# Kernel tuning notes

Measured on AMD Instinct MI355X. Metric: run time of the kernel, lower is better.

The kernel has to match this reference:

```python
import jax, jax.numpy as jnp
import numpy as np

N = 524288   # total graph nodes
V = 64       # number of virtual nodes (clusters)
C = N // V   # nodes per cluster (8192)
D = 256      # in_feats
H = 256      # hidden_feats
EPS = 1e-5


def setup_inputs() -> dict:
    key = jax.random.key(0)
    ks = jax.random.split(key, 8)
    sD = 1.0 / np.sqrt(D)
    sH = 1.0 / np.sqrt(2 * H)
    inp = {
        "x": jax.random.normal(ks[0], (N, D), dtype=jnp.float32),
        "vn_emb": jax.random.normal(ks[1], (V, D), dtype=jnp.float32) * 0.1,
        "wq": jax.random.normal(ks[2], (D, D), dtype=jnp.float32) * sD,
        "wk": jax.random.normal(ks[3], (D, D), dtype=jnp.float32) * sD,
        "v_attn": jax.random.normal(ks[4], (D,), dtype=jnp.float32) * sD,
        "w1": jax.random.normal(ks[5], (D, 2 * H), dtype=jnp.float32) * sD,
        "b1": jnp.zeros((2 * H,), dtype=jnp.float32),
        "g1": jnp.ones((2 * H,), dtype=jnp.float32),
        "beta1": jnp.zeros((2 * H,), dtype=jnp.float32),
        "w2": jax.random.normal(ks[6], (2 * H, H), dtype=jnp.float32) * sH,
        "b2": jnp.zeros((H,), dtype=jnp.float32),
        "g2": jnp.ones((H,), dtype=jnp.float32),
        "beta2": jnp.zeros((H,), dtype=jnp.float32),
        # cluster v owns contiguous node block [v*C, (v+1)*C)
        "vn_index": jnp.arange(N, dtype=jnp.int32).reshape(V, C),
        "vn_indices": jnp.stack(
            [jnp.arange(N, dtype=jnp.int32), (jnp.arange(N, dtype=jnp.int32) // C)],
            axis=1),
    }
    return inp


def _batchnorm(z, g, b):
    # training-mode BN over the virtual-node batch dim
    m = jnp.mean(z, axis=0)
    v = jnp.var(z, axis=0)
    return (z - m) * jax.lax.rsqrt(v + EPS) * g + b


def reference(x, vn_emb, wq, wk, v_attn, w1, b1, g1, beta1,
              w2, b2, g2, beta2, vn_index, vn_indices):
    vx = vn_emb                                   # [V, D]
    # --- update_node_emb (layer 0): broadcast-add VN emb to its nodes ---
    h = x + vx[vn_indices[:, 1]]                  # [N, D]
    # --- update_vn_emb: per-cluster additive attention pooling (vectorized over V) ---
    cluster_h = h[vn_index]                       # [V, C, D]
    q = vx @ wq                                   # [V, D]
    kproj = jnp.einsum('vcd,de->vce', cluster_h, wk)   # [V, C, D]
    scores = jnp.einsum('vce,e->vc', jnp.tanh(kproj + q[:, None, :]), v_attn)
    attn = jax.nn.softmax(scores, axis=-1)        # [V, C]
    pooled = jnp.einsum('vc,vcd->vd', attn, cluster_h) + vx  # [V, D]
    # --- mlp_vns[0]: Linear -> BN -> ReLU -> Linear -> BN -> ReLU ---
    z = jax.nn.relu(_batchnorm(pooled @ w1 + b1, g1, beta1))  # [V, 2H]
    vx_new = jax.nn.relu(_batchnorm(z @ w2 + b2, g2, beta2))  # [V, H]
    return h, vx_new
```

## Files before the change

### kernel.cpp

```cpp
#include <hip/hip_runtime.h>


typedef __bf16 bf16x8 __attribute__((ext_vector_type(8)));
typedef float f32x4 __attribute__((ext_vector_type(4)));
typedef unsigned short us8 __attribute__((ext_vector_type(8)));

__device__ __forceinline__ unsigned short f2bf(float f) {
  unsigned int u = __float_as_uint(f);
  return (unsigned short)((u + 0x7fffu + ((u >> 16) & 1u)) >> 16);
}
__device__ __forceinline__ float bf2f(unsigned short s) {
  return __uint_as_float(((unsigned int)s) << 16);
}
__device__ __forceinline__ float tanh_fast(float x) {
  float cx = fminf(fmaxf(x, -15.f), 15.f);
  float e = __expf(2.f * cx);
  return (e - 1.f) * __builtin_amdgcn_rcpf(e + 1.f);
}
__device__ __forceinline__ float wave_sum(float v) {
#pragma unroll
  for (int o = 1; o < 64; o <<= 1) v += __shfl_xor(v, o);
  return v;
}
__device__ __forceinline__ void lgkm_barrier() {
  asm volatile("s_waitcnt lgkmcnt(0)" ::: "memory");
  __builtin_amdgcn_sched_barrier(0);
  __builtin_amdgcn_s_barrier();
  __builtin_amdgcn_sched_barrier(0);
}

#define PXLD(dst, voff) \
  asm volatile("global_load_dwordx4 %0, %1, %2" : "=v"(dst) : "v"(voff), "s"(x))

__global__ __launch_bounds__(256) void k_prep(
    const float* __restrict__ vn_emb, const float* __restrict__ wq,
    const float* __restrict__ wk, float* __restrict__ qg,
    unsigned short* __restrict__ wkp) {
  int t = threadIdx.x;
  int b = blockIdx.x;
  if (b < 64) {
    float a = 0.f;
#pragma unroll 4
    for (int d = 0; d < 256; ++d) a += vn_emb[(b << 8) + d] * wq[(d << 8) + t];
    qg[(b << 8) + t] = a;
  } else {
    int tid = ((b - 64) << 8) + t;
    int l = tid & 63;
    int ks = (tid >> 6) & 7;
    int ct = tid >> 9;
    int col = (ct << 4) + (l & 15);
    int d0 = (ks << 5) + ((l >> 4) << 3);
    us8 o;
#pragma unroll
    for (int e = 0; e < 8; ++e) o[e] = f2bf(wk[(d0 + e) * 256 + col]);
    *reinterpret_cast<us8*>(wkp + (size_t)tid * 8) = o;
  }
}

__global__ __launch_bounds__(512, 2) void k_main(
    const float* __restrict__ x, const float* __restrict__ vn_emb,
    const float* __restrict__ v_attn, const float* __restrict__ qg,
    const unsigned short* __restrict__ wkp, float* __restrict__ hout,
    float* __restrict__ vecs, float* __restrict__ Zb) {
  __shared__ unsigned short wk_lds[65536];
  __shared__ unsigned short hs[32 * 256];
  __shared__ float vxs[256], qv[256], va[256];
  __shared__ float spbuf[4][32];

  const int t = threadIdx.x;
  const int blk = blockIdx.x;
  const int cl = blk >> 2;

  if (t < 256) {
    vxs[t] = vn_emb[(cl << 8) + t];
    qv[t] = qg[(cl << 8) + t];
    va[t] = v_attn[t];
  }
  {
    const f32x4* wkg = reinterpret_cast<const f32x4*>(wkp);
    f32x4* wkl = reinterpret_cast<f32x4*>(wk_lds);
#pragma unroll
    for (int j = 0; j < 16; ++j) wkl[(j << 9) + t] = wkg[(j << 9) + t];
  }

  const int l = t & 63, wv = t >> 6;
  const int lr = l & 15, lg = l >> 4;
  const int rg = wv & 1, ctq = wv >> 1;

  char* hsb = reinterpret_cast<char*>(hs);
  const unsigned blk_base = (unsigned)blk * 2097152u;
  f32x4* hop = reinterpret_cast<f32x4*>(hout) + ((size_t)blk << 17);

  f32x4 acc = {0.f, 0.f, 0.f, 0.f};
  float zacc = 0.f;

  f32x4 px0, px1, px2, px3;
  {
    unsigned vo = blk_base + ((unsigned)t << 4);
    PXLD(px0, vo);
    PXLD(px1, vo + 8192u);
    PXLD(px2, vo + 16384u);
    PXLD(px3, vo + 24576u);
  }
  __syncthreads();

  for (int tile = 0; tile < 64; ++tile) {
    asm volatile("s_waitcnt vmcnt(0)" ::: "memory");
    __builtin_amdgcn_sched_barrier(0);
    const int tb4 = tile << 11;
#define STAGE1_STEP(i, pxr)                                               \
  {                                                                       \
    int id = (i << 9) + t;                                                \
    int row = id >> 6, c4 = id & 63;                                      \
    f32x4 vv = *reinterpret_cast<const f32x4*>(&vxs[c4 << 2]);            \
    f32x4 hh = pxr + vv;                                                  \
    hop[tb4 + id] = hh;                                                   \
    ushort4 o;                                                            \
    o.x = f2bf(hh[0]);                                                    \
    o.y = f2bf(hh[1]);                                                    \
    o.z = f2bf(hh[2]);                                                    \
    o.w = f2bf(hh[3]);                                                    \
    *reinterpret_cast<ushort4*>(                                          \
        hsb + ((row << 9) + ((c4 << 3) ^ ((row & 7) << 4)))) = o;         \
  }
    STAGE1_STEP(0, px0)
    STAGE1_STEP(1, px1)
    STAGE1_STEP(2, px2)
    STAGE1_STEP(3, px3)
#undef STAGE1_STEP
    lgkm_barrier();

    if (tile < 63) {
      unsigned nvo = blk_base + ((unsigned)(tile + 1) << 15) + ((unsigned)t << 4);
      PXLD(px0, nvo);
      PXLD(px1, nvo + 8192u);
      PXLD(px2, nvo + 16384u);
      PXLD(px3, nvo + 24576u);
    }
    __builtin_amdgcn_sched_barrier(0);

    bf16x8 bfr[8];
    {
      int row2 = (rg << 4) + lr;
      int sw = (row2 & 7) << 4;
#pragma unroll
      for (int ks = 0; ks < 8; ++ks)
        bfr[ks] = __builtin_bit_cast(
            bf16x8, *reinterpret_cast<const us8*>(
                        hsb + ((row2 << 9) + ((((ks << 6) + (lg << 4))) ^ sw))));
    }
    float sp = 0.f;
#pragma unroll
    for (int c = 0; c < 4; ++c) {
      const int ct = (ctq << 2) + c;
      f32x4 ac0 = {0.f, 0.f, 0.f, 0.f};
#pragma unroll
      for (int ks = 0; ks < 8; ++ks) {
        bf16x8 af = __builtin_bit_cast(
            bf16x8, *reinterpret_cast<const us8*>(
                        wk_lds + ((size_t)(((ct << 3) + ks) << 6) + l) * 8));
        ac0 =
            __builtin_amdgcn_mfma_f32_16x16x32_bf16(af, bfr[ks], ac0, 0, 0, 0);
      }
      const int eo0 = (ct << 4) + (lg << 2);
      const f32x4 qf = *reinterpret_cast<const f32x4*>(&qv[eo0]);
      const f32x4 vf = *reinterpret_cast<const f32x4*>(&va[eo0]);
#pragma unroll
      for (int r = 0; r < 4; ++r) sp += tanh_fast(ac0[r] + qf[r]) * vf[r];
    }
    sp += __shfl_xor(sp, 16);
    sp += __shfl_xor(sp, 32);
    if (lg == 0) spbuf[ctq][(rg << 4) + lr] = sp;
    lgkm_barrier();

    float srow = 0.f;
    if (l < 32) srow = spbuf[0][l] + spbuf[1][l] + spbuf[2][l] + spbuf[3][l];
    float w_all = __expf(srow);
    if (wv == 0 && l < 32) zacc += w_all;

#pragma unroll
    for (int r = 0; r < 4; ++r) {
      int row = (wv << 2) + r;
      float wn = __shfl(w_all, row);
      ushort4 hv = *reinterpret_cast<const ushort4*>(
          hsb + ((row << 9) + ((l << 3) ^ ((row & 7) << 4))));
      acc[0] += wn * bf2f(hv.x);
      acc[1] += wn * bf2f(hv.y);
      acc[2] += wn * bf2f(hv.z);
      acc[3] += wn * bf2f(hv.w);
    }
    lgkm_barrier();
  }

  float* sc = reinterpret_cast<float*>(hs);
  *reinterpret_cast<f32x4*>(&sc[(wv << 8) + (l << 2)]) = acc;
  __syncthreads();
  if (t < 256) {
    float s = 0.f;
#pragma unroll
    for (int w8 = 0; w8 < 8; ++w8) s += sc[(w8 << 8) + t];
    vecs[((size_t)blk << 8) + t] = s;
  }
  if (wv == 0) {
    float z = wave_sum(zacc);
    if (l == 0) Zb[blk] = z;
  }
}

__global__ __launch_bounds__(256) void k_combine(
    const float* __restrict__ vecs, const float* __restrict__ Zb,
    const float* __restrict__ vn_emb, float* __restrict__ pooledT) {
  int v = blockIdx.x, t = threadIdx.x;
  float s = 0.f, z = 0.f;
#pragma unroll
  for (int b = 0; b < 4; ++b) {
    s += vecs[(size_t)(((v << 2) + b) << 8) + t];
    z += Zb[(v << 2) + b];
  }
  pooledT[(t << 6) + v] = s / z + vn_emb[(v << 8) + t];
}

__global__ __launch_bounds__(64) void k_mlp1(
    const float* __restrict__ pooledT, const float* __restrict__ w1,
    const float* __restrict__ b1, const float* __restrict__ g1,
    const float* __restrict__ be1, float* __restrict__ z1T) {
  int j = blockIdx.x, v = threadIdx.x;
  float a = 0.f;
#pragma unroll 4
  for (int d = 0; d < 256; ++d) a += pooledT[(d << 6) + v] * w1[(d << 9) + j];
  a += b1[j];
  float mu = wave_sum(a) * (1.f / 64.f);
  float df = a - mu;
  float var = wave_sum(df * df) * (1.f / 64.f);
  float z = df * rsqrtf(var + 1e-5f) * g1[j] + be1[j];
  z1T[(j << 6) + v] = fmaxf(z, 0.f);
}

__global__ __launch_bounds__(64) void k_mlp2(
    const float* __restrict__ z1T, const float* __restrict__ w2,
    const float* __restrict__ b2, const float* __restrict__ g2,
    const float* __restrict__ be2, float* __restrict__ vout) {
  int j = blockIdx.x, v = threadIdx.x;
  float a = 0.f;
#pragma unroll 4
  for (int k = 0; k < 512; ++k) a += z1T[(k << 6) + v] * w2[(k << 8) + j];
  a += b2[j];
  float mu = wave_sum(a) * (1.f / 64.f);
  float df = a - mu;
  float var = wave_sum(df * df) * (1.f / 64.f);
  float z = df * rsqrtf(var + 1e-5f) * g2[j] + be2[j];
  vout[(v << 8) + j] = fmaxf(z, 0.f);
}

extern "C" void kernel_launch(void* const* d_in, const int* in_sizes, int n_in,
                              void* d_out, int out_size, void* d_ws,
                              size_t ws_size, hipStream_t stream) {
  const float* x = (const float*)d_in[0];
  const float* vn_emb = (const float*)d_in[1];
  const float* wq = (const float*)d_in[2];
  const float* wk = (const float*)d_in[3];
  const float* v_attn = (const float*)d_in[4];
  const float* w1 = (const float*)d_in[5];
  const float* b1 = (const float*)d_in[6];
  const float* g1 = (const float*)d_in[7];
  const float* beta1 = (const float*)d_in[8];
  const float* w2 = (const float*)d_in[9];
  const float* b2 = (const float*)d_in[10];
  const float* g2 = (const float*)d_in[11];
  const float* beta2 = (const float*)d_in[12];

  char* wsb = (char*)d_ws;
  float* qg = (float*)(wsb + 0);
  unsigned short* wkp = (unsigned short*)(wsb + 65536);
  float* vecs = (float*)(wsb + 196608);
  float* Zb = (float*)(wsb + 458752);
  float* pooledT = (float*)(wsb + 462848);
  float* z1T = (float*)(wsb + 528384);

  float* hout = (float*)d_out;
  float* vout = hout + (size_t)524288 * 256;

  k_prep<<<96, 256, 0, stream>>>(vn_emb, wq, wk, qg, wkp);
  k_main<<<256, 512, 0, stream>>>(x, vn_emb, v_attn, qg, wkp, hout, vecs, Zb);
  k_combine<<<64, 256, 0, stream>>>(vecs, Zb, vn_emb, pooledT);
  k_mlp1<<<512, 64, 0, stream>>>(pooledT, w1, b1, g1, beta1, z1T);
  k_mlp2<<<256, 64, 0, stream>>>(z1T, w2, b2, g2, beta2, vout);
}
```

Measured before the change: 330.3 us.

## Stream x via global_load_lds double buffer, keep Wk fragments in registers

Loads of x now go straight into a two-deep LDS staging buffer through global_load_lds, prefetching two tiles ahead with a partial vmcnt wait instead of one tile ahead through registers. The bf16 Wk tile moves out of LDS into per-wave register fragments, which removes per-MFMA LDS reads. The pooling accumulation now uses the fp32 h values already held in registers rather than rereading bf16 h from LDS, which drops one barrier per tile. In exchange register pressure rises by 32 bf16x8 fragments per thread, which could limit occupancy or cause spills at 512 threads.

```diff
diff --git a/kernel.cpp b/kernel.cpp
--- a/kernel.cpp
+++ b/kernel.cpp
@@ -8,9 +8,6 @@
 __device__ __forceinline__ unsigned short f2bf(float f) {
   unsigned int u = __float_as_uint(f);
   return (unsigned short)((u + 0x7fffu + ((u >> 16) & 1u)) >> 16);
-}
-__device__ __forceinline__ float bf2f(unsigned short s) {
-  return __uint_as_float(((unsigned int)s) << 16);
 }
 __device__ __forceinline__ float tanh_fast(float x) {
   float cx = fminf(fmaxf(x, -15.f), 15.f);
@@ -28,9 +25,11 @@
   __builtin_amdgcn_s_barrier();
   __builtin_amdgcn_sched_barrier(0);
 }
-
-#define PXLD(dst, voff) \
-  asm volatile("global_load_dwordx4 %0, %1, %2" : "=v"(dst) : "v"(voff), "s"(x))
+__device__ __forceinline__ void gll16(const float* gp, float* lp) {
+  __builtin_amdgcn_global_load_lds(
+      (const __attribute__((address_space(1))) void*)gp,
+      (__attribute__((address_space(3))) void*)lp, 16, 0, 0);
+}
 
 __global__ __launch_bounds__(256) void k_prep(
     const float* __restrict__ vn_emb, const float* __restrict__ wq,
@@ -62,10 +61,10 @@
     const float* __restrict__ v_attn, const float* __restrict__ qg,
     const unsigned short* __restrict__ wkp, float* __restrict__ hout,
     float* __restrict__ vecs, float* __restrict__ Zb) {
-  __shared__ unsigned short wk_lds[65536];
+  __shared__ float stage[2][32 * 256];
   __shared__ unsigned short hs[32 * 256];
   __shared__ float vxs[256], qv[256], va[256];
-  __shared__ float spbuf[4][32];
+  __shared__ float spbuf[8][32];
 
   const int t = threadIdx.x;
   const int blk = blockIdx.x;
@@ -76,68 +75,78 @@
     qv[t] = qg[(cl << 8) + t];
     va[t] = v_attn[t];
   }
-  {
-    const f32x4* wkg = reinterpret_cast<const f32x4*>(wkp);
-    f32x4* wkl = reinterpret_cast<f32x4*>(wk_lds);
-#pragma unroll
-    for (int j = 0; j < 16; ++j) wkl[(j << 9) + t] = wkg[(j << 9) + t];
-  }
 
   const int l = t & 63, wv = t >> 6;
   const int lr = l & 15, lg = l >> 4;
   const int rg = wv & 1, ctq = wv >> 1;
 
+  bf16x8 wkf[4][8];
+#pragma unroll
+  for (int c = 0; c < 4; ++c)
+#pragma unroll
+    for (int ks = 0; ks < 8; ++ks) {
+      const int ct = (ctq << 2) + c;
+      wkf[c][ks] = __builtin_bit_cast(
+          bf16x8, *reinterpret_cast<const us8*>(
+                      wkp + ((size_t)((((ct << 3) + ks) << 6) + l)) * 8));
+    }
+
   char* hsb = reinterpret_cast<char*>(hs);
-  const unsigned blk_base = (unsigned)blk * 2097152u;
-  f32x4* hop = reinterpret_cast<f32x4*>(hout) + ((size_t)blk << 17);
+  const size_t growbase = ((size_t)blk << 11) + (wv << 2);
+  const int srow0 = wv << 2;
 
   f32x4 acc = {0.f, 0.f, 0.f, 0.f};
   float zacc = 0.f;
 
-  f32x4 px0, px1, px2, px3;
-  {
-    unsigned vo = blk_base + ((unsigned)t << 4);
-    PXLD(px0, vo);
-    PXLD(px1, vo + 8192u);
-    PXLD(px2, vo + 16384u);
-    PXLD(px3, vo + 24576u);
-  }
+#pragma unroll
+  for (int tt = 0; tt < 2; ++tt)
+#pragma unroll
+    for (int i = 0; i < 4; ++i)
+      gll16(x + (((growbase + (tt << 5) + i) << 8) + (l << 2)),
+            &stage[tt][(srow0 + i) << 8]);
+
   __syncthreads();
 
+  const f32x4 vv = *reinterpret_cast<const f32x4*>(&vxs[l << 2]);
+  f32x4 hh0, hh1, hh2, hh3;
+
   for (int tile = 0; tile < 64; ++tile) {
-    asm volatile("s_waitcnt vmcnt(0)" ::: "memory");
+    if (tile == 63) {
+      asm volatile("s_waitcnt vmcnt(0)" ::: "memory");
+    } else {
+      asm volatile("s_waitcnt vmcnt(4)" ::: "memory");
+    }
     __builtin_amdgcn_sched_barrier(0);
-    const int tb4 = tile << 11;
-#define STAGE1_STEP(i, pxr)                                               \
-  {                                                                       \
-    int id = (i << 9) + t;                                                \
-    int row = id >> 6, c4 = id & 63;                                      \
-    f32x4 vv = *reinterpret_cast<const f32x4*>(&vxs[c4 << 2]);            \
-    f32x4 hh = pxr + vv;                                                  \
-    hop[tb4 + id] = hh;                                                   \
-    ushort4 o;                                                            \
-    o.x = f2bf(hh[0]);                                                    \
-    o.y = f2bf(hh[1]);                                                    \
-    o.z = f2bf(hh[2]);                                                    \
-    o.w = f2bf(hh[3]);                                                    \
-    *reinterpret_cast<ushort4*>(                                          \
-        hsb + ((row << 9) + ((c4 << 3) ^ ((row & 7) << 4)))) = o;         \
-  }
-    STAGE1_STEP(0, px0)
-    STAGE1_STEP(1, px1)
-    STAGE1_STEP(2, px2)
-    STAGE1_STEP(3, px3)
-#undef STAGE1_STEP
+
+    const float* sb = &stage[tile & 1][0];
+    const size_t hg0 = ((growbase + ((size_t)tile << 5)) << 8) + (l << 2);
+#define S1(hhX, i)                                                          \
+  {                                                                         \
+    f32x4 sv = *reinterpret_cast<const f32x4*>(                             \
+        &sb[((srow0 + i) << 8) + (l << 2)]);                                \
+    hhX = sv + vv;                                                          \
+    *reinterpret_cast<f32x4*>(hout + hg0 + ((size_t)i << 8)) = hhX;         \
+    ushort4 o;                                                              \
+    o.x = f2bf(hhX[0]);                                                     \
+    o.y = f2bf(hhX[1]);                                                     \
+    o.z = f2bf(hhX[2]);                                                     \
+    o.w = f2bf(hhX[3]);                                                     \
+    int row = srow0 + i;                                                    \
+    *reinterpret_cast<ushort4*>(                                            \
+        hsb + ((row << 9) + ((l << 3) ^ ((row & 7) << 4)))) = o;            \
+  }
+    S1(hh0, 0) S1(hh1, 1) S1(hh2, 2) S1(hh3, 3)
+#undef S1
+
+    __builtin_amdgcn_sched_barrier(0);
+    if (tile < 62) {
+      const int tt = tile + 2;
+#pragma unroll
+      for (int i = 0; i < 4; ++i)
+        gll16(x + (((growbase + ((size_t)tt << 5) + i) << 8) + (l << 2)),
+              &stage[tile & 1][(srow0 + i) << 8]);
+    }
     lgkm_barrier();
-
-    if (tile < 63) {
-      unsigned nvo = blk_base + ((unsigned)(tile + 1) << 15) + ((unsigned)t << 4);
-      PXLD(px0, nvo);
-      PXLD(px1, nvo + 8192u);
-      PXLD(px2, nvo + 16384u);
-      PXLD(px3, nvo + 24576u);
-    }
-    __builtin_amdgcn_sched_barrier(0);
 
     bf16x8 bfr[8];
     {
@@ -155,13 +164,9 @@
       const int ct = (ctq << 2) + c;
       f32x4 ac0 = {0.f, 0.f, 0.f, 0.f};
 #pragma unroll
-      for (int ks = 0; ks < 8; ++ks) {
-        bf16x8 af = __builtin_bit_cast(
-            bf16x8, *reinterpret_cast<const us8*>(
-                        wk_lds + ((size_t)(((ct << 3) + ks) << 6) + l) * 8));
-        ac0 =
-            __builtin_amdgcn_mfma_f32_16x16x32_bf16(af, bfr[ks], ac0, 0, 0, 0);
-      }
+      for (int ks = 0; ks < 8; ++ks)
+        ac0 = __builtin_amdgcn_mfma_f32_16x16x32_bf16(wkf[c][ks], bfr[ks], ac0,
+                                                      0, 0, 0);
       const int eo0 = (ct << 4) + (lg << 2);
       const f32x4 qf = *reinterpret_cast<const f32x4*>(&qv[eo0]);
       const f32x4 vf = *reinterpret_cast<const f32x4*>(&va[eo0]);
@@ -170,28 +175,27 @@
     }
     sp += __shfl_xor(sp, 16);
     sp += __shfl_xor(sp, 32);
-    if (lg == 0) spbuf[ctq][(rg << 4) + lr] = sp;
+    if (lg == 0) spbuf[(ctq << 1) | rg][lr | (rg << 4)] = sp;
     lgkm_barrier();
 
     float srow = 0.f;
-    if (l < 32) srow = spbuf[0][l] + spbuf[1][l] + spbuf[2][l] + spbuf[3][l];
+    if (l < 32) {
+      int rh = l >> 4;
+#pragma unroll
+      for (int q = 0; q < 4; ++q) srow += spbuf[(q << 1) | rh][l];
+    }
     float w_all = __expf(srow);
     if (wv == 0 && l < 32) zacc += w_all;
-
-#pragma unroll
-    for (int r = 0; r < 4; ++r) {
-      int row = (wv << 2) + r;
-      float wn = __shfl(w_all, row);
-      ushort4 hv = *reinterpret_cast<const ushort4*>(
-          hsb + ((row << 9) + ((l << 3) ^ ((row & 7) << 4))));
-      acc[0] += wn * bf2f(hv.x);
-      acc[1] += wn * bf2f(hv.y);
-      acc[2] += wn * bf2f(hv.z);
-      acc[3] += wn * bf2f(hv.w);
-    }
-    lgkm_barrier();
-  }
-
+    {
+      float wn0 = __shfl(w_all, srow0 + 0);
+      float wn1 = __shfl(w_all, srow0 + 1);
+      float wn2 = __shfl(w_all, srow0 + 2);
+      float wn3 = __shfl(w_all, srow0 + 3);
+      acc += wn0 * hh0 + wn1 * hh1 + wn2 * hh2 + wn3 * hh3;
+    }
+  }
+
+  __syncthreads();
   float* sc = reinterpret_cast<float*>(hs);
   *reinterpret_cast<f32x4*>(&sc[(wv << 8) + (l << 2)]) = acc;
   __syncthreads();
```

Measured after the change: 325.8 us. Within noise of the previous version (-1.4%).
